# Kernel optimization log

Measured on AMD Instinct MI355X. Metric: run time of the kernel, lower is better.

The kernel has to match this reference:

```python
import jax, jax.numpy as jnp
import numpy as np

N = 1024
B = 32768


def _cc_mul(a, b):
    # complex multiply with real/imag stacked on axis 0; b broadcasts [2,N] against [2,B,N]
    real = a[0] * b[0] - a[1] * b[1]
    imag = a[0] * b[1] + a[1] * b[0]
    return jnp.stack((real, imag), axis=0)


def setup_inputs() -> dict:
    key = jax.random.key(0)
    k1, k2, k3, k4, k5 = jax.random.split(key, 5)
    x = jax.random.normal(k1, (2, B, N), dtype=jnp.float32)
    diag = jax.random.normal(k2, (2, N), dtype=jnp.float32)
    off_diag = jax.random.normal(k3, (2, N), dtype=jnp.float32)
    # pairwise swap permutation: (0,1),(2,3),... swapped -> 1,0,3,2,...
    pairwise = np.arange(N).reshape(-1, 2)[:, ::-1].ravel()
    pairwise_perm_idx = jnp.asarray(pairwise, dtype=jnp.int32)
    left_perm_idx = jax.random.permutation(k4, N).astype(jnp.int32)
    right_perm_idx = jax.random.permutation(k5, N).astype(jnp.int32)
    return {
        "x": x,
        "diag": diag,
        "off_diag": off_diag,
        "pairwise_perm_idx": pairwise_perm_idx,
        "left_perm_idx": left_perm_idx,
        "right_perm_idx": right_perm_idx,
    }


def reference(x, diag, off_diag, pairwise_perm_idx, left_perm_idx, right_perm_idx):
    # left permutation (gather on last dim)
    o = x[..., left_perm_idx]
    # diag path + pairwise-permuted off-diag path (complex MAC)
    out = _cc_mul(o, diag) + _cc_mul(o, off_diag)[..., pairwise_perm_idx]
    # right permutation
    return out[..., right_perm_idx]
```

## Files before the change

kernel.cpp:

```cpp
#include <hip/hip_runtime.h>


#define NCOLS 1024
#define TPB   256
#define KPT   4
#define BPB   16
#define NBUF  2

__global__ __launch_bounds__(TPB) void mesh_kernel(
    const float* __restrict__ x,
    const float* __restrict__ diag,
    const float* __restrict__ offd,
    const int*   __restrict__ pair,
    const int*   __restrict__ lperm,
    const int*   __restrict__ rperm,
    float* __restrict__ out,
    int B)
{
    __shared__ __align__(16) float smem[NBUF][2 * NCOLS];

    const int t = threadIdx.x;

    int   lr[KPT], lp[KPT];
    float d0[KPT], d1[KPT], f0[KPT], f1[KPT];
    const int4 rj = ((const int4*)rperm)[t];
    const int  rr[KPT] = {rj.x, rj.y, rj.z, rj.w};
#pragma unroll
    for (int k = 0; k < KPT; ++k) {
        const int r = rr[k];
        const int p = pair[r];
        lr[k] = lperm[r];
        lp[k] = lperm[p];
        d0[k] = diag[r];
        d1[k] = diag[NCOLS + r];
        f0[k] = offd[p];
        f1[k] = offd[NCOLS + p];
    }

    const long long BN = (long long)B * NCOLS;
    const int b0 = blockIdx.x * BPB;
    const int nb = min(BPB, B - b0);
    if (nb <= 0) return;

    const float4* g0 = (const float4*)(x + (long long)b0 * NCOLS);
    const float4* g1 = (const float4*)(x + BN + (long long)b0 * NCOLS);
    float* o0p = out + (long long)b0 * NCOLS;
    float* o1p = o0p + BN;
    const int RS4 = NCOLS / 4;

    float4 p0 = g0[t];
    float4 p1 = g1[t];
    ((float4*)smem[0])[t]           = p0;
    ((float4*)(smem[0] + NCOLS))[t] = p1;

    for (int i = 0; i < nb; ++i) {
        const bool pf = (i + 1 < nb);

        if (pf) {
            p0 = g0[(i + 1) * RS4 + t];
            p1 = g1[(i + 1) * RS4 + t];
        }

        __syncthreads();

        const float* sb = smem[i & 1];
        float4 q0, q1;
        float* q0a = (float*)&q0;
        float* q1a = (float*)&q1;
#pragma unroll
        for (int k = 0; k < KPT; ++k) {
            const float a0 = sb[lr[k]];
            const float a1 = sb[NCOLS + lr[k]];
            const float e0 = sb[lp[k]];
            const float e1 = sb[NCOLS + lp[k]];
            q0a[k] = a0 * d0[k] - a1 * d1[k] + e0 * f0[k] - e1 * f1[k];
            q1a[k] = a0 * d1[k] + a1 * d0[k] + e0 * f1[k] + e1 * f0[k];
        }
        ((float4*)(o0p + (long long)i * NCOLS))[t] = q0;
        ((float4*)(o1p + (long long)i * NCOLS))[t] = q1;

        if (pf) {
            float* nbuf = smem[(i + 1) & 1];
            ((float4*)nbuf)[t]           = p0;
            ((float4*)(nbuf + NCOLS))[t] = p1;
        }
    }
}

extern "C" void kernel_launch(void* const* d_in, const int* in_sizes, int n_in,
                              void* d_out, int out_size, void* d_ws, size_t ws_size,
                              hipStream_t stream) {
    const float* x     = (const float*)d_in[0];
    const float* diag  = (const float*)d_in[1];
    const float* offd  = (const float*)d_in[2];
    const int*   pair  = (const int*)d_in[3];
    const int*   lperm = (const int*)d_in[4];
    const int*   rperm = (const int*)d_in[5];
    float* out = (float*)d_out;

    const int N = in_sizes[1] / 2;
    const int B = in_sizes[0] / (2 * N);
    (void)N;

    dim3 grid((B + BPB - 1) / BPB);
    mesh_kernel<<<grid, TPB, 0, stream>>>(x, diag, offd, pair, lperm, rperm, out, B);
}
```

Baseline: 447.0 us.

## Precompute permuted indices and coefficients, interleave real/imag in swizzled shared memory

Adds a small setup kernel that writes pre-composed permutation indices and permuted diag/off-diagonal coefficients to workspace, so the main kernel loads them as vectors instead of doing dependent scalar gathers. Shared memory now holds real and imag interleaved with an XOR swizzle, so each gather is one 8-byte LDS read instead of two. Global loads and stores become nontemporal, and rows per block drop from 16 to 4 for more blocks. The original kernel is kept as a fallback when no workspace is available. The cost is an extra kernel launch and more per-block setup overhead.

```diff
diff --git a/kernel.cpp b/kernel.cpp
--- a/kernel.cpp
+++ b/kernel.cpp
@@ -4,23 +4,126 @@
 #define NCOLS 1024
 #define TPB   256
 #define KPT   4
-#define BPB   16
+#define BPB   4
 #define NBUF  2
+#define WS_BYTES (6 * NCOLS * 4)
+
+typedef float vf4 __attribute__((ext_vector_type(4)));
+typedef float vf2 __attribute__((ext_vector_type(2)));
+typedef int   vi4 __attribute__((ext_vector_type(4)));
+
+__global__ __launch_bounds__(TPB) void setup_kernel(
+    const float* __restrict__ diag, const float* __restrict__ offd,
+    const int* __restrict__ pair, const int* __restrict__ lperm,
+    const int* __restrict__ rperm, int* __restrict__ ws)
+{
+    const int j = blockIdx.x * TPB + threadIdx.x;
+    if (j >= NCOLS) return;
+    const int r = rperm[j];
+    const int p = pair[r];
+    int*   s0 = ws;
+    int*   s1 = ws + NCOLS;
+    float* cf = (float*)(ws + 2 * NCOLS);
+    s0[j]             = lperm[r];
+    s1[j]             = lperm[p];
+    cf[j]             = diag[r];
+    cf[NCOLS + j]     = diag[NCOLS + r];
+    cf[2 * NCOLS + j] = offd[p];
+    cf[3 * NCOLS + j] = offd[NCOLS + p];
+}
+
+__device__ __forceinline__ int swz(int byteoff) {
+    return byteoff ^ (((byteoff >> 7) & 1) << 4);
+}
 
 __global__ __launch_bounds__(TPB) void mesh_kernel(
     const float* __restrict__ x,
-    const float* __restrict__ diag,
-    const float* __restrict__ offd,
-    const int*   __restrict__ pair,
-    const int*   __restrict__ lperm,
-    const int*   __restrict__ rperm,
+    const int*   __restrict__ ws,
     float* __restrict__ out,
     int B)
 {
+    __shared__ __align__(16) char smem[NBUF][8 * NCOLS];
+
+    const int t = threadIdx.x;
+
+    const vi4 s0v = ((const vi4*)ws)[t];
+    const vi4 s1v = ((const vi4*)(ws + NCOLS))[t];
+    const float* cf = (const float*)(ws + 2 * NCOLS);
+    const vf4 D0 = ((const vf4*)cf)[t];
+    const vf4 D1 = ((const vf4*)(cf + NCOLS))[t];
+    const vf4 F0 = ((const vf4*)(cf + 2 * NCOLS))[t];
+    const vf4 F1 = ((const vf4*)(cf + 3 * NCOLS))[t];
+
+    const long long BN = (long long)B * NCOLS;
+    const int b0 = blockIdx.x * BPB;
+    const int nb = min(BPB, B - b0);
+    if (nb <= 0) return;
+
+    const vf4* g0 = (const vf4*)(x + (long long)b0 * NCOLS);
+    const vf4* g1 = (const vf4*)(x + BN + (long long)b0 * NCOLS);
+    float* o0p = out + (long long)b0 * NCOLS;
+    float* o1p = o0p + BN;
+    const int RS4 = NCOLS / 4;
+
+    vf4 p0 = __builtin_nontemporal_load(g0 + t);
+    vf4 p1 = __builtin_nontemporal_load(g1 + t);
+    {
+        char* sb = smem[0];
+        vf4 w0; w0.x = p0.x; w0.y = p1.x; w0.z = p0.y; w0.w = p1.y;
+        vf4 w1; w1.x = p0.z; w1.y = p1.z; w1.z = p0.w; w1.w = p1.w;
+        *(vf4*)(sb + swz(32 * t))      = w0;
+        *(vf4*)(sb + swz(32 * t + 16)) = w1;
+    }
+
+    for (int i = 0; i < nb; ++i) {
+        const bool pf = (i + 1 < nb);
+        if (pf) {
+            p0 = __builtin_nontemporal_load(g0 + (i + 1) * RS4 + t);
+            p1 = __builtin_nontemporal_load(g1 + (i + 1) * RS4 + t);
+        }
+        __syncthreads();
+
+        const char* sb = smem[i & 1];
+        vf4 q0, q1;
+#pragma unroll
+        for (int k = 0; k < KPT; ++k) {
+            const int lrk = (k == 0) ? s0v.x : (k == 1) ? s0v.y : (k == 2) ? s0v.z : s0v.w;
+            const int lpk = (k == 0) ? s1v.x : (k == 1) ? s1v.y : (k == 2) ? s1v.z : s1v.w;
+            const float d0k = (k == 0) ? D0.x : (k == 1) ? D0.y : (k == 2) ? D0.z : D0.w;
+            const float d1k = (k == 0) ? D1.x : (k == 1) ? D1.y : (k == 2) ? D1.z : D1.w;
+            const float f0k = (k == 0) ? F0.x : (k == 1) ? F0.y : (k == 2) ? F0.z : F0.w;
+            const float f1k = (k == 0) ? F1.x : (k == 1) ? F1.y : (k == 2) ? F1.z : F1.w;
+            const vf2 a = *(const vf2*)(sb + swz(8 * lrk));
+            const vf2 e = *(const vf2*)(sb + swz(8 * lpk));
+            const float r0 = a.x * d0k - a.y * d1k + e.x * f0k - e.y * f1k;
+            const float r1 = a.x * d1k + a.y * d0k + e.x * f1k + e.y * f0k;
+            if (k == 0) { q0.x = r0; q1.x = r1; }
+            else if (k == 1) { q0.y = r0; q1.y = r1; }
+            else if (k == 2) { q0.z = r0; q1.z = r1; }
+            else { q0.w = r0; q1.w = r1; }
+        }
+        __builtin_nontemporal_store(q0, (vf4*)(o0p + (long long)i * NCOLS) + t);
+        __builtin_nontemporal_store(q1, (vf4*)(o1p + (long long)i * NCOLS) + t);
+
+        if (pf) {
+            char* nbf = smem[(i + 1) & 1];
+            vf4 w0; w0.x = p0.x; w0.y = p1.x; w0.z = p0.y; w0.w = p1.y;
+            vf4 w1; w1.x = p0.z; w1.y = p1.z; w1.z = p0.w; w1.w = p1.w;
+            *(vf4*)(nbf + swz(32 * t))      = w0;
+            *(vf4*)(nbf + swz(32 * t + 16)) = w1;
+        }
+    }
+}
+
+#define FB_BPB 16
+__global__ __launch_bounds__(TPB) void mesh_kernel_fb(
+    const float* __restrict__ x, const float* __restrict__ diag,
+    const float* __restrict__ offd, const int* __restrict__ pair,
+    const int* __restrict__ lperm, const int* __restrict__ rperm,
+    float* __restrict__ out, int B)
+{
     __shared__ __align__(16) float smem[NBUF][2 * NCOLS];
-
     const int t = threadIdx.x;
-
     int   lr[KPT], lp[KPT];
     float d0[KPT], d1[KPT], f0[KPT], f1[KPT];
     const int4 rj = ((const int4*)rperm)[t];
@@ -29,40 +132,27 @@
     for (int k = 0; k < KPT; ++k) {
         const int r = rr[k];
         const int p = pair[r];
-        lr[k] = lperm[r];
-        lp[k] = lperm[p];
-        d0[k] = diag[r];
-        d1[k] = diag[NCOLS + r];
-        f0[k] = offd[p];
-        f1[k] = offd[NCOLS + p];
-    }
-
+        lr[k] = lperm[r];  lp[k] = lperm[p];
+        d0[k] = diag[r];   d1[k] = diag[NCOLS + r];
+        f0[k] = offd[p];   f1[k] = offd[NCOLS + p];
+    }
     const long long BN = (long long)B * NCOLS;
-    const int b0 = blockIdx.x * BPB;
-    const int nb = min(BPB, B - b0);
+    const int b0 = blockIdx.x * FB_BPB;
+    const int nb = min(FB_BPB, B - b0);
     if (nb <= 0) return;
-
     const float4* g0 = (const float4*)(x + (long long)b0 * NCOLS);
     const float4* g1 = (const float4*)(x + BN + (long long)b0 * NCOLS);
     float* o0p = out + (long long)b0 * NCOLS;
     float* o1p = o0p + BN;
     const int RS4 = NCOLS / 4;
-
     float4 p0 = g0[t];
     float4 p1 = g1[t];
     ((float4*)smem[0])[t]           = p0;
     ((float4*)(smem[0] + NCOLS))[t] = p1;
-
     for (int i = 0; i < nb; ++i) {
         const bool pf = (i + 1 < nb);
-
-        if (pf) {
-            p0 = g0[(i + 1) * RS4 + t];
-            p1 = g1[(i + 1) * RS4 + t];
-        }
-
+        if (pf) { p0 = g0[(i + 1) * RS4 + t]; p1 = g1[(i + 1) * RS4 + t]; }
         __syncthreads();
-
         const float* sb = smem[i & 1];
         float4 q0, q1;
         float* q0a = (float*)&q0;
@@ -78,11 +168,10 @@
         }
         ((float4*)(o0p + (long long)i * NCOLS))[t] = q0;
         ((float4*)(o1p + (long long)i * NCOLS))[t] = q1;
-
         if (pf) {
-            float* nbuf = smem[(i + 1) & 1];
-            ((float4*)nbuf)[t]           = p0;
-            ((float4*)(nbuf + NCOLS))[t] = p1;
+            float* nbf = smem[(i + 1) & 1];
+            ((float4*)nbf)[t]           = p0;
+            ((float4*)(nbf + NCOLS))[t] = p1;
         }
     }
 }
@@ -102,6 +191,15 @@
     const int B = in_sizes[0] / (2 * N);
     (void)N;
 
-    dim3 grid((B + BPB - 1) / BPB);
-    mesh_kernel<<<grid, TPB, 0, stream>>>(x, diag, offd, pair, lperm, rperm, out, B);
-}
+    if (d_ws != nullptr && ws_size >= (size_t)WS_BYTES) {
+        int* ws = (int*)d_ws;
+        setup_kernel<<<dim3(NCOLS / TPB), TPB, 0, stream>>>(diag, offd, pair,
+                                                            lperm, rperm, ws);
+        dim3 grid((B + BPB - 1) / BPB);
+        mesh_kernel<<<grid, TPB, 0, stream>>>(x, ws, out, B);
+    } else {
+        dim3 grid((B + FB_BPB - 1) / FB_BPB);
+        mesh_kernel_fb<<<grid, TPB, 0, stream>>>(x, diag, offd, pair, lperm,
+                                                 rperm, out, B);
+    }
+}
```

After: 432.2 us. 3.3% less time.
